# Kernel tuning notes

Hardware: AMD Instinct MI355X
Metric: run time of the kernel (lower is better)

## Reference

```python
import jax, jax.numpy as jnp
import numpy as np

DIM = 1024
DEPTH = 6
HEADS = 16
MLP = 4096
HEAD_DIM = DIM // HEADS
SCALE = HEAD_DIM ** -0.5
EPS = 1e-5


def _ln(x, g, b):
    m = jnp.mean(x, axis=-1, keepdims=True)
    v = jnp.mean(jnp.square(x - m), axis=-1, keepdims=True)
    return (x - m) * jax.lax.rsqrt(v + EPS) * g + b


def setup_inputs() -> dict:
    key = jax.random.key(0)
    ks = jax.random.split(key, 16)
    B, N = 4, 1024
    s_d = 1.0 / np.sqrt(DIM)
    s_m = 1.0 / np.sqrt(MLP)
    inp = {
        "x1": jax.random.normal(ks[0], (B, N, DIM), jnp.float32),
        "x2": jax.random.normal(ks[1], (B, N, DIM), jnp.float32),
        # stacked per-layer params; Linear weights stored as [in, out]
        "ln1_g": jnp.ones((DEPTH, DIM), jnp.float32),
        "ln1_b": jnp.zeros((DEPTH, DIM), jnp.float32),
        "wq": jax.random.normal(ks[2], (DEPTH, DIM, DIM), jnp.float32) * s_d,
        "wk": jax.random.normal(ks[3], (DEPTH, DIM, DIM), jnp.float32) * s_d,
        "wv": jax.random.normal(ks[4], (DEPTH, DIM, DIM), jnp.float32) * s_d,
        "wo": jax.random.normal(ks[5], (DEPTH, DIM, DIM), jnp.float32) * s_d,
        "bo": jnp.zeros((DEPTH, DIM), jnp.float32),
        "ln2_g": jnp.ones((DEPTH, DIM), jnp.float32),
        "ln2_b": jnp.zeros((DEPTH, DIM), jnp.float32),
        "w1": jax.random.normal(ks[6], (DEPTH, DIM, MLP), jnp.float32) * s_d,
        "b1": jnp.zeros((DEPTH, MLP), jnp.float32),
        "w2": jax.random.normal(ks[7], (DEPTH, MLP, DIM), jnp.float32) * s_m,
        "b2": jnp.zeros((DEPTH, DIM), jnp.float32),
    }
    return inp


def _split_heads(t):
    b, n, _ = t.shape
    return t.reshape(b, n, HEADS, HEAD_DIM).transpose(0, 2, 1, 3)  # b h n d


def reference(x1, x2, ln1_g, ln1_b, wq, wk, wv, wo, bo, ln2_g, ln2_b, w1, b1, w2, b2):
    # dropout disabled (eval mode)
    for i in range(DEPTH):
        # PreNorm(MCA): same LayerNorm params applied to x1 and x2
        n1 = _ln(x1, ln1_g[i], ln1_b[i])
        n2 = _ln(x2, ln1_g[i], ln1_b[i])
        q = _split_heads(n1 @ wq[i])
        k = _split_heads(n2 @ wk[i])
        v = _split_heads(n2 @ wv[i])
        dots = jnp.einsum('bhqd,bhkd->bhqk', q, k) * SCALE
        attn = jax.nn.softmax(dots, axis=-1)
        out = jnp.einsum('bhqk,bhkd->bhqd', attn, v)
        b, h, n, d = out.shape
        out = out.transpose(0, 2, 1, 3).reshape(b, n, h * d)
        x1 = out @ wo[i] + bo[i] + x1
        # PreNorm(FeedForward)
        nf = _ln(x1, ln2_g[i], ln2_b[i])
        hdn = jax.nn.gelu(nf @ w1[i] + b1[i], approximate=False)
        x1 = hdn @ w2[i] + b2[i] + x1
    return x1
```

## Files before the change

### kernel.cpp

```cpp
#include <hip/hip_runtime.h>
#include <stdint.h>

#define N_SEQ 1024
#define N_TOK 4096
#define ATT_SCALE 0.125f

typedef unsigned short u16;
typedef __attribute__((ext_vector_type(8))) short short8;
typedef __attribute__((ext_vector_type(4))) short short4v;
typedef __attribute__((ext_vector_type(4))) float f32x4;

__device__ __forceinline__ u16 f2bf(float f) {
  uint32_t u = __float_as_uint(f);
  u += 0x7fffu + ((u >> 16) & 1u);
  return (u16)(u >> 16);
}

__device__ __forceinline__ void gload16(const void* g, void* lds) {
  __builtin_amdgcn_global_load_lds(
      (const __attribute__((address_space(1))) unsigned int*)g,
      (__attribute__((address_space(3))) unsigned int*)lds, 16, 0, 0);
}

__global__ void copy_f32_kernel(const float* __restrict__ in, float* __restrict__ out) {
  int i = blockIdx.x * 256 + threadIdx.x;
  ((float4*)out)[i] = ((const float4*)in)[i];
}

__global__ __launch_bounds__(256) void tconv_kernel(const float* __restrict__ src,
                                                    u16* __restrict__ dst,
                                                    int K, int NN, size_t dstLS) {
  __shared__ u16 tile[64][68];
  int n0 = blockIdx.x * 64, k0 = blockIdx.y * 64, L = blockIdx.z;
  const float* s = src + (size_t)L * K * NN;
  u16* d = dst + (size_t)L * dstLS;
  int t = threadIdx.x;
  int rr = t >> 4, cc = (t & 15) * 4;
#pragma unroll
  for (int ii = 0; ii < 4; ii++) {
    int kl = rr + ii * 16;
    float4 v = *(const float4*)&s[(size_t)(k0 + kl) * NN + n0 + cc];
    tile[cc + 0][kl] = f2bf(v.x);
    tile[cc + 1][kl] = f2bf(v.y);
    tile[cc + 2][kl] = f2bf(v.z);
    tile[cc + 3][kl] = f2bf(v.w);
  }
  __syncthreads();
#pragma unroll
  for (int ii = 0; ii < 4; ii++) {
    int nl = rr + ii * 16;
    short4v o;
    o.x = (short)tile[nl][cc + 0];
    o.y = (short)tile[nl][cc + 1];
    o.z = (short)tile[nl][cc + 2];
    o.w = (short)tile[nl][cc + 3];
    *(short4v*)&d[(size_t)(n0 + nl) * K + k0 + cc] = o;
  }
}

__global__ __launch_bounds__(256) void ln_kernel(const float* __restrict__ x,
                                                 const float* __restrict__ g,
                                                 const float* __restrict__ b,
                                                 u16* __restrict__ out) {
  int row = blockIdx.x;
  const float* xr = x + (size_t)row * 1024;
  int t = threadIdx.x;
  float4 v = *(const float4*)&xr[t * 4];
  float s = v.x + v.y + v.z + v.w;
  float sq = v.x * v.x + v.y * v.y + v.z * v.z + v.w * v.w;
#pragma unroll
  for (int m = 1; m < 64; m <<= 1) {
    s += __shfl_xor(s, m, 64);
    sq += __shfl_xor(sq, m, 64);
  }
  __shared__ float ps[8];
  int w = t >> 6;
  if ((t & 63) == 0) { ps[w] = s; ps[4 + w] = sq; }
  __syncthreads();
  s = ps[0] + ps[1] + ps[2] + ps[3];
  sq = ps[4] + ps[5] + ps[6] + ps[7];
  float mean = s * (1.0f / 1024.0f);
  float var = sq * (1.0f / 1024.0f) - mean * mean;
  float rs = rsqrtf(var + 1e-5f);
  float4 gv = *(const float4*)&g[t * 4];
  float4 bv = *(const float4*)&b[t * 4];
  short4v o;
  o.x = (short)f2bf((v.x - mean) * rs * gv.x + bv.x);
  o.y = (short)f2bf((v.y - mean) * rs * gv.y + bv.y);
  o.z = (short)f2bf((v.z - mean) * rs * gv.z + bv.z);
  o.w = (short)f2bf((v.w - mean) * rs * gv.w + bv.w);
  *(short4v*)&out[(size_t)row * 1024 + t * 4] = o;
}

template <int BM, int BN, int WM, int WN, int MAXB, int MODE>
__global__ __launch_bounds__(WM * WN * 64, MAXB) void gemmS(const u16* __restrict__ A,
                                                            const u16* __restrict__ Bt,
                                                            u16* __restrict__ outb,
                                                            float* __restrict__ outf,
                                                            const float* __restrict__ bias,
                                                            const float* __restrict__ resid,
                                                            int N, int K) {
  constexpr int BK = 64;
  constexpr int NW = WM * WN;
  constexpr int T = NW * 64;
  constexpr int WTM = BM / WM, WTN = BN / WN;
  constexpr int FM = WTM / 16, FN = WTN / 16;
  constexpr int AT = BM * BK, BTL = BN * BK;
  constexpr int LA = AT / 8 / T, LB = BTL / 8 / T;
  __shared__ u16 smem[2 * (AT + BTL)];

  int t = threadIdx.x, lane = t & 63, w = t >> 6;
  int wm = w / WN, wn = w % WN;
  const u16* Ag = A + (size_t)(blockIdx.y * BM) * K;
  const u16* Bg = Bt + (size_t)(blockIdx.x * BN) * K;
  f32x4 acc[FM][FN] = {};

  auto stage = [&](int d, int k0) {
    u16* ab = smem + d * (AT + BTL);
    u16* bb = ab + AT;
#pragma unroll
    for (int l = 0; l < LA; l++) {
      int c = (l * NW + w) * 64 + lane;
      int r = c >> 3, s = c & 7;
      gload16(Ag + (size_t)r * K + k0 + ((s ^ (r & 7)) << 3), ab + (l * NW + w) * 512);
    }
#pragma unroll
    for (int l = 0; l < LB; l++) {
      int c = (l * NW + w) * 64 + lane;
      int r = c >> 3, s = c & 7;
      gload16(Bg + (size_t)r * K + k0 + ((s ^ (r & 7)) << 3), bb + (l * NW + w) * 512);
    }
  };

  auto rdA = [&](const u16* ab, int mi, int ks) {
    int rr = wm * WTM + mi * 16 + (lane & 15);
    int j = ks * 4 + (lane >> 4);
    return *(const short8*)&ab[rr * BK + ((j ^ (rr & 7)) << 3)];
  };
  auto rdB = [&](const u16* bb, int ni, int ks) {
    int rr = wn * WTN + ni * 16 + (lane & 15);
    int j = ks * 4 + (lane >> 4);
    return *(const short8*)&bb[rr * BK + ((j ^ (rr & 7)) << 3)];
  };

  const int NT = K / BK;
  stage(0, 0);
  __syncthreads();

  int buf = 0;
  for (int tt = 0; tt < NT; tt++) {
    if (tt + 1 < NT) stage(buf ^ 1, (tt + 1) * BK);
    const u16* ab = smem + buf * (AT + BTL);
    const u16* bb = ab + AT;
    short8 af[2][FM], bfr[2][FN];
#pragma unroll
    for (int ks = 0; ks < 2; ks++) {
#pragma unroll
      for (int mi = 0; mi < FM; mi++) af[ks][mi] = rdA(ab, mi, ks);
#pragma unroll
      for (int ni = 0; ni < FN; ni++) bfr[ks][ni] = rdB(bb, ni, ks);
    }
#pragma unroll
    for (int ks = 0; ks < 2; ks++)
#pragma unroll
      for (int mi = 0; mi < FM; mi++)
#pragma unroll
        for (int ni = 0; ni < FN; ni++)
          acc[mi][ni] = __builtin_amdgcn_mfma_f32_16x16x32_bf16(af[ks][mi], bfr[ks][ni],
                                                                acc[mi][ni], 0, 0, 0);
    __syncthreads();
    buf ^= 1;
  }

  int r0 = blockIdx.y * BM + wm * WTM + ((lane >> 4) << 2);
  int c0 = blockIdx.x * BN + wn * WTN + (lane & 15);
#pragma unroll
  for (int mi = 0; mi < FM; mi++) {
#pragma unroll
    for (int r = 0; r < 4; r++) {
      size_t row = (size_t)(r0 + mi * 16 + r);
#pragma unroll
      for (int ni = 0; ni < FN; ni++) {
        size_t col = (size_t)(c0 + ni * 16);
        size_t idx = row * N + col;
        float val = acc[mi][ni][r];
        if (MODE == 0) {
          outb[idx] = f2bf(val);
        } else if (MODE == 1) {
          outf[idx] = val + bias[col] + resid[idx];
        } else {
          float xg = val + bias[col];
          outb[idx] = f2bf(0.5f * xg * (1.0f + erff(xg * 0.70710678f)));
        }
      }
    }
  }
}

__global__ __launch_bounds__(256, 4) void attn_kernel(const u16* __restrict__ qb,
                                                      const u16* __restrict__ kvb,
                                                      u16* __restrict__ ob) {
  int qt = blockIdx.x, bh = blockIdx.y;
  int b = bh >> 4, h = bh & 15;
  int t = threadIdx.x, lane = t & 63, w = t >> 6;
  __shared__ u16 Qs[64 * 64];
  __shared__ u16 Ks[64 * 64];
  __shared__ u16 Vt[64 * 64];
  __shared__ u16 Ps[4][16 * 64];

  const u16* qbase = qb + (size_t)b * N_SEQ * 1024 + h * 64;
  const u16* kbase = kvb + (size_t)b * N_SEQ * 2048 + h * 64;
  const u16* vbase = kbase + 1024;
  u16* obase = ob + (size_t)b * N_SEQ * 1024 + h * 64;

  int r = t >> 2, c = (t & 3) * 16;
  {
    const u16* src = qbase + (size_t)(qt * 64 + r) * 1024 + c;
    *(short8*)&Qs[r * 64 + c] = *(const short8*)src;
    *(short8*)&Qs[r * 64 + c + 8] = *(const short8*)(src + 8);
  }
  short8 kreg0, kreg1, vreg0, vreg1;
  {
    const u16* ksrc = kbase + (size_t)r * 2048 + c;
    kreg0 = *(const short8*)ksrc;
    kreg1 = *(const short8*)(ksrc + 8);
    const u16* vsrc = vbase + (size_t)r * 2048 + c;
    vreg0 = *(const short8*)vsrc;
    vreg1 = *(const short8*)(vsrc + 8);
  }
  __syncthreads();
  short8 qa0 = *(const short8*)&Qs[(w * 16 + (lane & 15)) * 64 + (lane >> 4) * 8];
  short8 qa1 = *(const short8*)&Qs[(w * 16 + (lane & 15)) * 64 + 32 + (lane >> 4) * 8];

  f32x4 o[4] = {};
  float m_r[4] = {-1e30f, -1e30f, -1e30f, -1e30f};
  float l_r[4] = {0.0f, 0.0f, 0.0f, 0.0f};

  for (int kt = 0; kt < 16; kt++) {
    if (kt > 0) __syncthreads();
    {
      int jj0 = c >> 3;
      *(short8*)&Ks[r * 64 + ((jj0 ^ (r & 7)) << 3)] = kreg0;
      *(short8*)&Ks[r * 64 + (((jj0 + 1) ^ (r & 7)) << 3)] = kreg1;
#pragma unroll
      for (int j = 0; j < 8; j++) {
        int row = c + j, rowb = c + 8 + j;
        Vt[row * 64 + (((r >> 3) ^ (row & 7)) << 3) + (r & 7)] = (u16)vreg0[j];
        Vt[rowb * 64 + (((r >> 3) ^ (rowb & 7)) << 3) + (r & 7)] = (u16)vreg1[j];
      }
    }
    __syncthreads();
    if (kt < 15) {
      const u16* ksrc = kbase + (size_t)((kt + 1) * 64 + r) * 2048 + c;
      kreg0 = *(const short8*)ksrc;
      kreg1 = *(const short8*)(ksrc + 8);
      const u16* vsrc = vbase + (size_t)((kt + 1) * 64 + r) * 2048 + c;
      vreg0 = *(const short8*)vsrc;
      vreg1 = *(const short8*)(vsrc + 8);
    }

    f32x4 s[4] = {};
#pragma unroll
    for (int kb = 0; kb < 4; kb++) {
      int key = kb * 16 + (lane & 15);
      int jj = lane >> 4;
      short8 k0 = *(const short8*)&Ks[key * 64 + ((jj ^ (key & 7)) << 3)];
      short8 k1 = *(const short8*)&Ks[key * 64 + (((4 + jj) ^ (key & 7)) << 3)];
      s[kb] = __builtin_amdgcn_mfma_f32_16x16x32_bf16(qa0, k0, s[kb], 0, 0, 0);
      s[kb] = __builtin_amdgcn_mfma_f32_16x16x32_bf16(qa1, k1, s[kb], 0, 0, 0);
    }
    float fac[4], rowsum[4];
#pragma unroll
    for (int rr = 0; rr < 4; rr++) {
      float a = fmaxf(fmaxf(s[0][rr], s[1][rr]), fmaxf(s[2][rr], s[3][rr])) * ATT_SCALE;
      a = fmaxf(a, __shfl_xor(a, 1, 64));
      a = fmaxf(a, __shfl_xor(a, 2, 64));
      a = fmaxf(a, __shfl_xor(a, 4, 64));
      a = fmaxf(a, __shfl_xor(a, 8, 64));
      float mn = fmaxf(m_r[rr], a);
      fac[rr] = __expf(m_r[rr] - mn);
      m_r[rr] = mn;
      rowsum[rr] = 0.0f;
    }
#pragma unroll
    for (int kb = 0; kb < 4; kb++) {
      int chunk = 2 * kb + ((lane & 15) >> 3);
#pragma unroll
      for (int rr = 0; rr < 4; rr++) {
        float p = __expf(s[kb][rr] * ATT_SCALE - m_r[rr]);
        rowsum[rr] += p;
        int row = (lane >> 4) * 4 + rr;
        Ps[w][row * 64 + ((chunk ^ (row & 7)) << 3) + (lane & 7)] = f2bf(p);
      }
    }
#pragma unroll
    for (int rr = 0; rr < 4; rr++) {
      float rs = rowsum[rr];
      rs += __shfl_xor(rs, 1, 64);
      rs += __shfl_xor(rs, 2, 64);
      rs += __shfl_xor(rs, 4, 64);
      rs += __shfl_xor(rs, 8, 64);
      l_r[rr] = l_r[rr] * fac[rr] + rs;
      o[0][rr] *= fac[rr];
      o[1][rr] *= fac[rr];
      o[2][rr] *= fac[rr];
      o[3][rr] *= fac[rr];
    }
#pragma unroll
    for (int ks = 0; ks < 2; ks++) {
      int rowp = lane & 15;
      int jj = 4 * ks + (lane >> 4);
      short8 pf = *(const short8*)&Ps[w][rowp * 64 + ((jj ^ (rowp & 7)) << 3)];
#pragma unroll
      for (int db = 0; db < 4; db++) {
        int row = db * 16 + (lane & 15);
        short8 vf = *(const short8*)&Vt[row * 64 + ((jj ^ (row & 7)) << 3)];
        o[db] = __builtin_amdgcn_mfma_f32_16x16x32_bf16(pf, vf, o[db], 0, 0, 0);
      }
    }
  }
#pragma unroll
  for (int rr = 0; rr < 4; rr++) {
    float inv = 1.0f / l_r[rr];
    size_t row = (size_t)(qt * 64 + w * 16 + (lane >> 4) * 4 + rr);
#pragma unroll
    for (int db = 0; db < 4; db++)
      obase[row * 1024 + db * 16 + (lane & 15)] = f2bf(o[db][rr] * inv);
  }
}

extern "C" void kernel_launch(void* const* d_in, const int* in_sizes, int n_in,
                              void* d_out, int out_size, void* d_ws, size_t ws_size,
                              hipStream_t stream) {
  const float* x1 = (const float*)d_in[0];
  const float* x2 = (const float*)d_in[1];
  const float* ln1_g = (const float*)d_in[2];
  const float* ln1_b = (const float*)d_in[3];
  const float* wq = (const float*)d_in[4];
  const float* wk = (const float*)d_in[5];
  const float* wv = (const float*)d_in[6];
  const float* wo = (const float*)d_in[7];
  const float* bo = (const float*)d_in[8];
  const float* ln2_g = (const float*)d_in[9];
  const float* ln2_b = (const float*)d_in[10];
  const float* w1 = (const float*)d_in[11];
  const float* b1 = (const float*)d_in[12];
  const float* w2 = (const float*)d_in[13];
  const float* b2 = (const float*)d_in[14];
  float* xout = (float*)d_out;

  u16* p = (u16*)d_ws;
  u16* wqt = p;  p += (size_t)6 * 1024 * 1024;
  u16* kvt = p;  p += (size_t)6 * 2048 * 1024;
  u16* wot = p;  p += (size_t)6 * 1024 * 1024;
  u16* w1t = p;  p += (size_t)6 * 4096 * 1024;
  u16* w2t = p;  p += (size_t)6 * 1024 * 4096;
  u16* n1 = p;   p += (size_t)N_TOK * 1024;
  u16* n2 = p;   p += (size_t)N_TOK * 1024;
  u16* qbuf = p; p += (size_t)N_TOK * 1024;
  u16* kvbuf = p; p += (size_t)N_TOK * 2048;
  u16* ao = p;   p += (size_t)N_TOK * 1024;
  u16* hid = p;  p += (size_t)N_TOK * 4096;

  dim3 blk(256);
  tconv_kernel<<<dim3(16, 16, 6), blk, 0, stream>>>(wq, wqt, 1024, 1024, (size_t)1024 * 1024);
  tconv_kernel<<<dim3(16, 16, 6), blk, 0, stream>>>(wk, kvt, 1024, 1024, (size_t)2048 * 1024);
  tconv_kernel<<<dim3(16, 16, 6), blk, 0, stream>>>(wv, kvt + (size_t)1024 * 1024, 1024, 1024, (size_t)2048 * 1024);
  tconv_kernel<<<dim3(16, 16, 6), blk, 0, stream>>>(wo, wot, 1024, 1024, (size_t)1024 * 1024);
  tconv_kernel<<<dim3(64, 16, 6), blk, 0, stream>>>(w1, w1t, 1024, 4096, (size_t)4096 * 1024);
  tconv_kernel<<<dim3(16, 64, 6), blk, 0, stream>>>(w2, w2t, 4096, 1024, (size_t)1024 * 4096);
  copy_f32_kernel<<<4096, blk, 0, stream>>>(x1, xout);

  for (int i = 0; i < 6; i++) {
    ln_kernel<<<N_TOK, blk, 0, stream>>>(xout, ln1_g + i * 1024, ln1_b + i * 1024, n1);
    ln_kernel<<<N_TOK, blk, 0, stream>>>(x2, ln1_g + i * 1024, ln1_b + i * 1024, n2);
    gemmS<64, 64, 2, 2, 4, 0><<<dim3(16, 64), dim3(256), 0, stream>>>(
        n1, wqt + (size_t)i * 1024 * 1024, qbuf, nullptr, nullptr, nullptr, 1024, 1024);
    gemmS<64, 128, 2, 2, 3, 0><<<dim3(16, 64), dim3(256), 0, stream>>>(
        n2, kvt + (size_t)i * 2048 * 1024, kvbuf, nullptr, nullptr, nullptr, 2048, 1024);
    attn_kernel<<<dim3(16, 64), blk, 0, stream>>>(qbuf, kvbuf, ao);
    gemmS<64, 64, 2, 2, 4, 1><<<dim3(16, 64), dim3(256), 0, stream>>>(
        ao, wot + (size_t)i * 1024 * 1024, nullptr, xout, bo + i * 1024, xout, 1024, 1024);
    ln_kernel<<<N_TOK, blk, 0, stream>>>(xout, ln2_g + i * 1024, ln2_b + i * 1024, n1);
    gemmS<64, 128, 2, 2, 3, 2><<<dim3(32, 64), dim3(256), 0, stream>>>(
        n1, w1t + (size_t)i * 4096 * 1024, hid, nullptr, b1 + i * 4096, nullptr, 4096, 1024);
    gemmS<64, 64, 2, 2, 4, 1><<<dim3(16, 64), dim3(256), 0, stream>>>(
        hid, w2t + (size_t)i * 1024 * 4096, nullptr, xout, b2 + i * 1024, xout, 1024, 4096);
  }
}
```

Before: 1.691 ms.

## Hoist x2 K/V projections out of layer loop into one batched GEMM

K and V depend only on x2 and per-layer LN params, so the LayerNorms of x2 for all six layers are computed up front. A single z-batched GEMM (grid z=6) then produces all K/V projections at once, giving a larger launch with better occupancy and fewer launches inside the loop. The Q, output-projection and FFN-down GEMMs also switch from 64x64 to 64x128 tiles, which halves their block counts. This needs extra workspace for six normalized copies and six KV buffers.

```diff
diff --git a/kernel.cpp b/kernel.cpp
--- a/kernel.cpp
+++ b/kernel.cpp
@@ -99,7 +99,8 @@
                                                             float* __restrict__ outf,
                                                             const float* __restrict__ bias,
                                                             const float* __restrict__ resid,
-                                                            int N, int K) {
+                                                            int N, int K,
+                                                            size_t zA, size_t zB, size_t zC) {
   constexpr int BK = 64;
   constexpr int NW = WM * WN;
   constexpr int T = NW * 64;
@@ -111,8 +112,9 @@
 
   int t = threadIdx.x, lane = t & 63, w = t >> 6;
   int wm = w / WN, wn = w % WN;
-  const u16* Ag = A + (size_t)(blockIdx.y * BM) * K;
-  const u16* Bg = Bt + (size_t)(blockIdx.x * BN) * K;
+  size_t z = blockIdx.z;
+  const u16* Ag = A + z * zA + (size_t)(blockIdx.y * BM) * K;
+  const u16* Bg = Bt + z * zB + (size_t)(blockIdx.x * BN) * K;
   f32x4 acc[FM][FN] = {};
 
   auto stage = [&](int d, int k0) {
@@ -182,7 +184,7 @@
 #pragma unroll
       for (int ni = 0; ni < FN; ni++) {
         size_t col = (size_t)(c0 + ni * 16);
-        size_t idx = row * N + col;
+        size_t idx = z * zC + row * N + col;
         float val = acc[mi][ni][r];
         if (MODE == 0) {
           outb[idx] = f2bf(val);
@@ -350,17 +352,17 @@
   float* xout = (float*)d_out;
 
   u16* p = (u16*)d_ws;
-  u16* wqt = p;  p += (size_t)6 * 1024 * 1024;
-  u16* kvt = p;  p += (size_t)6 * 2048 * 1024;
-  u16* wot = p;  p += (size_t)6 * 1024 * 1024;
-  u16* w1t = p;  p += (size_t)6 * 4096 * 1024;
-  u16* w2t = p;  p += (size_t)6 * 1024 * 4096;
-  u16* n1 = p;   p += (size_t)N_TOK * 1024;
-  u16* n2 = p;   p += (size_t)N_TOK * 1024;
-  u16* qbuf = p; p += (size_t)N_TOK * 1024;
-  u16* kvbuf = p; p += (size_t)N_TOK * 2048;
-  u16* ao = p;   p += (size_t)N_TOK * 1024;
-  u16* hid = p;  p += (size_t)N_TOK * 4096;
+  u16* wqt = p;   p += (size_t)6 * 1024 * 1024;
+  u16* kvt = p;   p += (size_t)6 * 2048 * 1024;
+  u16* wot = p;   p += (size_t)6 * 1024 * 1024;
+  u16* w1t = p;   p += (size_t)6 * 4096 * 1024;
+  u16* w2t = p;   p += (size_t)6 * 1024 * 4096;
+  u16* n1 = p;    p += (size_t)N_TOK * 1024;
+  u16* n2all = p; p += (size_t)6 * N_TOK * 1024;
+  u16* qbuf = p;  p += (size_t)N_TOK * 1024;
+  u16* kvb6 = p;  p += (size_t)6 * N_TOK * 2048;
+  u16* ao = p;    p += (size_t)N_TOK * 1024;
+  u16* hid = p;   p += (size_t)N_TOK * 4096;
 
   dim3 blk(256);
   tconv_kernel<<<dim3(16, 16, 6), blk, 0, stream>>>(wq, wqt, 1024, 1024, (size_t)1024 * 1024);
@@ -371,20 +373,24 @@
   tconv_kernel<<<dim3(16, 64, 6), blk, 0, stream>>>(w2, w2t, 4096, 1024, (size_t)1024 * 4096);
   copy_f32_kernel<<<4096, blk, 0, stream>>>(x1, xout);
 
+  for (int i = 0; i < 6; i++)
+    ln_kernel<<<N_TOK, blk, 0, stream>>>(x2, ln1_g + i * 1024, ln1_b + i * 1024,
+                                         n2all + (size_t)i * N_TOK * 1024);
+  gemmS<64, 128, 2, 2, 3, 0><<<dim3(16, 64, 6), blk, 0, stream>>>(
+      n2all, kvt, kvb6, nullptr, nullptr, nullptr, 2048, 1024,
+      (size_t)N_TOK * 1024, (size_t)2048 * 1024, (size_t)N_TOK * 2048);
+
   for (int i = 0; i < 6; i++) {
     ln_kernel<<<N_TOK, blk, 0, stream>>>(xout, ln1_g + i * 1024, ln1_b + i * 1024, n1);
-    ln_kernel<<<N_TOK, blk, 0, stream>>>(x2, ln1_g + i * 1024, ln1_b + i * 1024, n2);
-    gemmS<64, 64, 2, 2, 4, 0><<<dim3(16, 64), dim3(256), 0, stream>>>(
-        n1, wqt + (size_t)i * 1024 * 1024, qbuf, nullptr, nullptr, nullptr, 1024, 1024);
-    gemmS<64, 128, 2, 2, 3, 0><<<dim3(16, 64), dim3(256), 0, stream>>>(
-        n2, kvt + (size_t)i * 2048 * 1024, kvbuf, nullptr, nullptr, nullptr, 2048, 1024);
-    attn_kernel<<<dim3(16, 64), blk, 0, stream>>>(qbuf, kvbuf, ao);
-    gemmS<64, 64, 2, 2, 4, 1><<<dim3(16, 64), dim3(256), 0, stream>>>(
-        ao, wot + (size_t)i * 1024 * 1024, nullptr, xout, bo + i * 1024, xout, 1024, 1024);
+    gemmS<64, 128, 2, 2, 3, 0><<<dim3(8, 64), blk, 0, stream>>>(
+        n1, wqt + (size_t)i * 1024 * 1024, qbuf, nullptr, nullptr, nullptr, 1024, 1024, 0, 0, 0);
+    attn_kernel<<<dim3(16, 64), blk, 0, stream>>>(qbuf, kvb6 + (size_t)i * N_TOK * 2048, ao);
+    gemmS<64, 128, 2, 2, 3, 1><<<dim3(8, 64), blk, 0, stream>>>(
+        ao, wot + (size_t)i * 1024 * 1024, nullptr, xout, bo + i * 1024, xout, 1024, 1024, 0, 0, 0);
     ln_kernel<<<N_TOK, blk, 0, stream>>>(xout, ln2_g + i * 1024, ln2_b + i * 1024, n1);
-    gemmS<64, 128, 2, 2, 3, 2><<<dim3(32, 64), dim3(256), 0, stream>>>(
-        n1, w1t + (size_t)i * 4096 * 1024, hid, nullptr, b1 + i * 4096, nullptr, 4096, 1024);
-    gemmS<64, 64, 2, 2, 4, 1><<<dim3(16, 64), dim3(256), 0, stream>>>(
-        hid, w2t + (size_t)i * 1024 * 4096, nullptr, xout, b2 + i * 1024, xout, 1024, 4096);
-  }
-}
+    gemmS<64, 128, 2, 2, 3, 2><<<dim3(32, 64), blk, 0, stream>>>(
+        n1, w1t + (size_t)i * 4096 * 1024, hid, nullptr, b1 + i * 4096, nullptr, 4096, 1024, 0, 0, 0);
+    gemmS<64, 128, 2, 2, 3, 1><<<dim3(8, 64), blk, 0, stream>>>(
+        hid, w2t + (size_t)i * 1024 * 4096, nullptr, xout, b2 + i * 1024, xout, 1024, 4096, 0, 0, 0);
+  }
+}
```

After: 1.726 ms. +2.0%, slower.
